# Kernel tuning notes

Hardware: AMD Instinct MI355X
Metric: run time of the kernel (lower is better)

Reference implementation:

```python
import jax, jax.numpy as jnp
import numpy as np

B, M, K, F, H = 4096, 50000, 31, 256, 256
N = K + 1                      # nodes per graph: center + K neighbors
GAMMA = 1.0 / (2.0 * 1.0 ** 2) # rbf_kernel gamma with length_scale = 1.0


def setup_inputs() -> dict:
    key = jax.random.key(0)
    k = jax.random.split(key, 9)
    return {
        "spatial_features": jax.random.normal(k[0], (B, 2), jnp.float32),
        "features": jax.random.normal(k[1], (B, F), jnp.float32),
        "train_spatial": jax.random.normal(k[2], (M, 2), jnp.float32),
        "train_features": jax.random.normal(k[3], (M, F), jnp.float32),
        "train_y": jax.random.normal(k[4], (M, 1), jnp.float32),
        "W0": jax.random.normal(k[5], (F + 2, H), jnp.float32) * (1.0 / np.sqrt(F + 2)),
        "W1": jax.random.normal(k[6], (H, H), jnp.float32) * (1.0 / np.sqrt(H)),
        "W2": jax.random.normal(k[7], (H, H), jnp.float32) * (1.0 / np.sqrt(H)),
        "Wout": jax.random.normal(k[8], (H, 1), jnp.float32) * (1.0 / np.sqrt(H)),
    }


def reference(spatial_features, features, train_spatial, train_features, train_y,
              W0, W1, W2, Wout):
    # --- brute-force kNN over train spatial coords (sklearn kneighbors) ---
    d2 = (jnp.sum(spatial_features ** 2, -1, keepdims=True)
          - 2.0 * spatial_features @ train_spatial.T
          + jnp.sum(train_spatial ** 2, -1)[None, :])                 # [B, M]
    nb = jax.lax.top_k(jax.lax.stop_gradient(-d2), K)[1]              # [B, K] indices

    # --- form_input_graph: node features = [feat ++ y ++ indicator] ---
    feat = jnp.concatenate([features[:, None, :], train_features[nb]], axis=1)    # [B,N,F]
    y = jnp.concatenate([jnp.zeros((B, 1, 1), feat.dtype), train_y[nb]], axis=1)  # [B,N,1]
    ind = jnp.zeros((B, N, 1), feat.dtype).at[:, 0, 0].set(1.0)                   # [B,N,1]
    x = jnp.concatenate([feat, y, ind], axis=-1)                                  # [B,N,F+2]

    # --- dense RBF adjacency: complete graph, self-loops already on diagonal ---
    coords = jnp.concatenate([spatial_features[:, None, :], train_spatial[nb]], axis=1)  # [B,N,2]
    diff = coords[:, :, None, :] - coords[:, None, :, :]
    A = jnp.exp(-GAMMA * jnp.sum(diff * diff, -1))                    # [B,N,N]
    # GCN symmetric normalization D^-1/2 A D^-1/2 (deg > 0 since diag = 1)
    dinv = jax.lax.rsqrt(jnp.sum(A, -1))                              # [B,N]
    Ahat = A * dinv[:, :, None] * dinv[:, None, :]

    h = jax.nn.relu(jnp.einsum('bij,bjh->bih', Ahat, x @ W0))
    h = jax.nn.relu(jnp.einsum('bij,bjh->bih', Ahat, h @ W1))
    h = jax.nn.relu(jnp.einsum('bij,bjh->bih', Ahat, h @ W2))

    # center node -> linear head (bias=False), last_activation='none'
    return h[:, 0] @ Wout                                             # [B, 1]
```

## Files before the change

kernel.cpp:

```cpp
#include <hip/hip_runtime.h>

typedef _Float16 half8 __attribute__((ext_vector_type(8)));
typedef float f32x16 __attribute__((ext_vector_type(16)));

#define M_TRAIN 50000
#define NQ 4096
#define KNN 31

#define LO_SCALE 1024.0f
#define LO_INV   9.765625e-4f

__global__ void prep_weights_k(const float* __restrict__ W0,
                               const float* __restrict__ W1,
                               const float* __restrict__ W2,
                               _Float16* __restrict__ W0hi, _Float16* __restrict__ W0lo,
                               _Float16* __restrict__ W1hi, _Float16* __restrict__ W1lo,
                               _Float16* __restrict__ W2hi, _Float16* __restrict__ W2lo) {
    int t = blockIdx.x * 256 + threadIdx.x;
    const int n0 = 17 * 8 * 64, n1 = 16 * 8 * 64, n2 = 16 * 8 * 64;
    if (t >= n0 + n1 + n2) return;
    const float* src; _Float16 *dhi, *dlo; int idx, Kin;
    if (t < n0)           { src = W0; dhi = W0hi; dlo = W0lo; idx = t;           Kin = 258; }
    else if (t < n0 + n1) { src = W1; dhi = W1hi; dlo = W1lo; idx = t - n0;      Kin = 256; }
    else                  { src = W2; dhi = W2hi; dlo = W2lo; idx = t - n0 - n1; Kin = 256; }
    int lane = idx & 63, nt = (idx >> 6) & 7, ks = idx >> 9;
    int col = nt * 32 + (lane & 31);
    int k0  = ks * 16 + (lane >> 5) * 8;
    _Float16 vhi[8], vlo[8];
#pragma unroll
    for (int j = 0; j < 8; j++) {
        int k = k0 + j;
        float w = (k < Kin) ? src[k * 256 + col] : 0.f;
        _Float16 hi = (_Float16)w;
        vhi[j] = hi;
        vlo[j] = (_Float16)((w - (float)hi) * LO_SCALE);
    }
    *reinterpret_cast<uint4*>(dhi + (size_t)idx * 8) = *reinterpret_cast<const uint4*>(vhi);
    *reinterpret_cast<uint4*>(dlo + (size_t)idx * 8) = *reinterpret_cast<const uint4*>(vlo);
}

#define QPB2 4
#define TILE2 2048
#define CAP2 128

__global__ __launch_bounds__(256) void knn_k(const float* __restrict__ qs,
                                             const float* __restrict__ ts,
                                             int* __restrict__ nb) {
    __shared__ __align__(16) float tile[TILE2 * 2];
    __shared__ float  mrg[QPB2][128];
    __shared__ int    ci[QPB2][CAP2];
    __shared__ double chd[QPB2][CAP2];
    __shared__ int    cnt[QPB2];

    const int t = threadIdx.x;
    const int w = t >> 6, lane = t & 63;
    const int q = blockIdx.x * QPB2 + w;

    if (lane == 0) cnt[w] = 0;
    const float qx = qs[q * 2 + 0], qy = qs[q * 2 + 1];

    float v0 = 3.4e38f, v1 = 3.4e38f;
    for (int base = 0; base < M_TRAIN; base += TILE2) {
        const int n = min(TILE2, M_TRAIN - base);
        __syncthreads();
        for (int i = t; i < n / 2; i += 256)
            reinterpret_cast<float4*>(tile)[i] =
                reinterpret_cast<const float4*>(ts + (size_t)base * 2)[i];
        __syncthreads();
#pragma unroll 4
        for (int p = lane; p < n; p += 64) {
            float dx = qx - tile[2 * p], dy = qy - tile[2 * p + 1];
            float d2 = dx * dx + dy * dy;
            if (d2 < v1) { if (d2 < v0) { v1 = v0; v0 = d2; } else v1 = d2; }
        }
    }
    __syncthreads();
    mrg[w][2 * lane]     = v0;
    mrg[w][2 * lane + 1] = v1;
    __syncthreads();

    float xa = mrg[w][lane], xb = mrg[w][64 + lane];
    int lea = 0, leb = 0;
    for (int i = 0; i < 128; i++) {
        float v = mrg[w][i];
        lea += (v <= xa) ? 1 : 0;
        leb += (v <= xb) ? 1 : 0;
    }
    float tc = 3.4e38f;
    if (lea >= 31) tc = xa;
    if (leb >= 31 && xb < tc) tc = xb;
#pragma unroll
    for (int off = 32; off; off >>= 1)
        tc = fminf(tc, __shfl_xor(tc, off));
    const float thr = tc * 1.00001f + 1e-7f;

    for (int base = 0; base < M_TRAIN; base += TILE2) {
        const int n = min(TILE2, M_TRAIN - base);
        __syncthreads();
        for (int i = t; i < n / 2; i += 256)
            reinterpret_cast<float4*>(tile)[i] =
                reinterpret_cast<const float4*>(ts + (size_t)base * 2)[i];
        __syncthreads();
#pragma unroll 4
        for (int p = lane; p < n; p += 64) {
            float dx = qx - tile[2 * p], dy = qy - tile[2 * p + 1];
            float d2 = dx * dx + dy * dy;
            if (d2 < thr) {
                int pos = atomicAdd(&cnt[w], 1);
                if (pos < CAP2) ci[w][pos] = base + p;
            }
        }
    }
    __syncthreads();

    const int C = min(cnt[w], CAP2);
    for (int c = lane; c < C; c += 64) {
        int idx = ci[w][c];
        double dx = (double)qx - (double)ts[idx * 2];
        double dy = (double)qy - (double)ts[idx * 2 + 1];
        chd[w][c] = dx * dx + dy * dy;
    }
    __syncthreads();
    for (int c = lane; c < C; c += 64) {
        double key = chd[w][c];
        int   idx = ci[w][c];
        int rank = 0;
        for (int o = 0; o < C; o++) {
            double ok = chd[w][o];
            int    oi = ci[w][o];
            rank += ((ok < key) || (ok == key && oi < idx)) ? 1 : 0;
        }
        if (rank < KNN) nb[q * KNN + rank] = idx;
    }
}

#define PX 276
#define PT 36

__device__ inline half8 ld_h8(const _Float16* p) {
    union { half8 h; uint2 u[2]; } r;
    r.u[0] = *reinterpret_cast<const uint2*>(p);
    r.u[1] = *reinterpret_cast<const uint2*>(p + 4);
    return r.h;
}
__device__ inline half8 ld_h8_g(const _Float16* p) {
    union { half8 h; uint4 u; } r;
    r.u = *reinterpret_cast<const uint4*>(p);
    return r.h;
}
__device__ inline f32x16 zero16() {
    f32x16 z;
#pragma unroll
    for (int i = 0; i < 16; i++) z[i] = 0.f;
    return z;
}
__device__ inline unsigned packh(_Float16 a, _Float16 b) {
    union { _Float16 f[2]; unsigned u; } p;
    p.f[0] = a; p.f[1] = b;
    return p.u;
}
__device__ inline half8 frag_x(const unsigned* w, int ks2, int h) {
    unsigned w0 = w[4 * ks2 + 0], w1 = w[4 * ks2 + 1];
    unsigned w2 = w[4 * ks2 + 2], w3 = w[4 * ks2 + 3];
    unsigned sA = h ? w0 : w2, sB = h ? w1 : w3;
    unsigned rA = __shfl_xor(sA, 32);
    unsigned rB = __shfl_xor(sB, 32);
    unsigned kA = h ? w2 : w0, kB = h ? w3 : w1;
    union { half8 h8; unsigned u[4]; } f;
    f.u[0] = h ? rA : kA;
    f.u[1] = h ? rB : kB;
    f.u[2] = h ? kA : rA;
    f.u[3] = h ? kB : rB;
    return f.h8;
}
#define MFMA(a, b, c) __builtin_amdgcn_mfma_f32_32x32x16_f16((a), (b), (c), 0, 0, 0)

__global__ __launch_bounds__(256, 4) void gcn_k(
    const float* __restrict__ qs, const float* __restrict__ qf,
    const float* __restrict__ ts, const float* __restrict__ tf,
    const float* __restrict__ ty, const float* __restrict__ Wout,
    const int* __restrict__ nb,
    const _Float16* __restrict__ W0hi, const _Float16* __restrict__ W0lo,
    const _Float16* __restrict__ W1hi, const _Float16* __restrict__ W1lo,
    const _Float16* __restrict__ W2hi, const _Float16* __restrict__ W2lo,
    float* __restrict__ out) {
    __shared__ __align__(16) _Float16 Xhi[32 * PX];
    __shared__ __align__(16) _Float16 Xlo[32 * PX];
    __shared__ _Float16 Ahhi[32 * PT];
    __shared__ _Float16 Ahlo[32 * PT];
    __shared__ float coords[64];
    __shared__ float dinv[32];
    __shared__ float yvs[32];
    __shared__ int   idxs[32];

    const int t = threadIdx.x;
    const int w = t >> 6, lane = t & 63;
    const int h = lane >> 5, ln = lane & 31;
    const int q0 = blockIdx.x;

    if (t < 32) {
        int idx = (t == 0) ? -1 : nb[q0 * KNN + (t - 1)];
        idxs[t] = idx;
        const float* c = (t == 0) ? (qs + (size_t)q0 * 2) : (ts + (size_t)idx * 2);
        coords[t * 2 + 0] = c[0];
        coords[t * 2 + 1] = c[1];
        yvs[t] = (t == 0) ? 0.f : ty[idx];
    }
    __syncthreads();

    {
        const float* src0 = (w == 0) ? (qf + (size_t)q0 * 256)
                                     : (tf + (size_t)idxs[w] * 256);
        float4 pv = reinterpret_cast<const float4*>(src0)[lane];
        for (int r = w; r < 32; r += 4) {
            float4 cv = pv;
            int rn = r + 4;
            if (rn < 32)
                pv = reinterpret_cast<const float4*>(tf + (size_t)idxs[rn] * 256)[lane];
            float a4[4] = {cv.x, cv.y, cv.z, cv.w};
            _Float16 hi4[4], lo4[4];
#pragma unroll
            for (int j = 0; j < 4; j++) {
                _Float16 hi = (_Float16)a4[j];
                hi4[j] = hi;
                lo4[j] = (_Float16)((a4[j] - (float)hi) * LO_SCALE);
            }
            *reinterpret_cast<uint2*>(&Xhi[r * PX + 4 * lane]) = *reinterpret_cast<uint2*>(hi4);
            *reinterpret_cast<uint2*>(&Xlo[r * PX + 4 * lane]) = *reinterpret_cast<uint2*>(lo4);
            if (lane == 0) {
                float yv = yvs[r];
                _Float16 thi[16], tlo[16];
#pragma unroll
                for (int j = 0; j < 16; j++) { thi[j] = (_Float16)0.f; tlo[j] = (_Float16)0.f; }
                _Float16 yh = (_Float16)yv;
                thi[0] = yh;
                tlo[0] = (_Float16)((yv - (float)yh) * LO_SCALE);
                thi[1] = (r == 0) ? (_Float16)1.f : (_Float16)0.f;
#pragma unroll
                for (int c = 0; c < 4; c++) {
                    *reinterpret_cast<uint2*>(&Xhi[r * PX + 256 + 4 * c]) = reinterpret_cast<uint2*>(thi)[c];
                    *reinterpret_cast<uint2*>(&Xlo[r * PX + 256 + 4 * c]) = reinterpret_cast<uint2*>(tlo)[c];
                }
            }
        }
    }

    if (t < 64) {
        int i = t >> 1, jh = t & 1;
        float xi = coords[i * 2], yi = coords[i * 2 + 1];
        float part = 0.f;
#pragma unroll
        for (int jj = 0; jj < 16; jj++) {
            int j = jh * 16 + jj;
            float dx = xi - coords[j * 2], dy = yi - coords[j * 2 + 1];
            part += __expf(-0.5f * (dx * dx + dy * dy));
        }
        float asum = part + __shfl_xor(part, 1);
        if (jh == 0) dinv[i] = 1.0f / sqrtf(asum);
    }
    __syncthreads();
    if (t < 64) {
        int i = t >> 1, jh = t & 1;
        float xi = coords[i * 2], yi = coords[i * 2 + 1];
        float di = dinv[i];
        _Float16 ahi[16], alo[16];
#pragma unroll
        for (int jj = 0; jj < 16; jj++) {
            int j = jh * 16 + jj;
            float dx = xi - coords[j * 2], dy = yi - coords[j * 2 + 1];
            float a = __expf(-0.5f * (dx * dx + dy * dy)) * di * dinv[j];
            _Float16 hi = (_Float16)a;
            ahi[jj] = hi;
            alo[jj] = (_Float16)((a - (float)hi) * LO_SCALE);
        }
        _Float16* dh = &Ahhi[i * PT + jh * 16];
        _Float16* dl = &Ahlo[i * PT + jh * 16];
#pragma unroll
        for (int c = 0; c < 4; c++) {
            reinterpret_cast<uint2*>(dh)[c] = reinterpret_cast<uint2*>(ahi)[c];
            reinterpret_cast<uint2*>(dl)[c] = reinterpret_cast<uint2*>(alo)[c];
        }
    }
    __syncthreads();

    const _Float16* Whis[3] = {W0hi, W1hi, W2hi};
    const _Float16* Wlos[3] = {W0lo, W1lo, W2lo};
    for (int layer = 0; layer < 3; layer++) {
        const _Float16* Whi = Whis[layer];
        const _Float16* Wlo = Wlos[layer];
        const int KS = (layer == 0) ? 17 : 16;

        f32x16 acc0 = zero16(), acc1 = zero16();
        f32x16 cor0 = zero16(), cor1 = zero16();
        size_t bo = ((size_t)(2 * w) * 64 + lane) * 8;
        half8 cAhi = ld_h8(&Xhi[ln * PX + 8 * h]);
        half8 cAlo = ld_h8(&Xlo[ln * PX + 8 * h]);
        half8 cBh0 = ld_h8_g(Whi + bo);
        half8 cBh1 = ld_h8_g(Whi + bo + 512);
        half8 cBl0 = ld_h8_g(Wlo + bo);
        half8 cBl1 = ld_h8_g(Wlo + bo + 512);
#pragma unroll 4
        for (int ks = 0; ks < KS; ks++) {
            half8 nAhi, nAlo, nBh0, nBh1, nBl0, nBl1;
            const bool more = (ks + 1 < KS);
            if (more) {
                size_t nbo = bo + 4096;
                nAhi = ld_h8(&Xhi[ln * PX + (ks + 1) * 16 + 8 * h]);
                nAlo = ld_h8(&Xlo[ln * PX + (ks + 1) * 16 + 8 * h]);
                nBh0 = ld_h8_g(Whi + nbo);
                nBh1 = ld_h8_g(Whi + nbo + 512);
                nBl0 = ld_h8_g(Wlo + nbo);
                nBl1 = ld_h8_g(Wlo + nbo + 512);
            }
            acc0 = MFMA(cAhi, cBh0, acc0);
            cor0 = MFMA(cAlo, cBh0, cor0);
            cor0 = MFMA(cAhi, cBl0, cor0);
            acc1 = MFMA(cAhi, cBh1, acc1);
            cor1 = MFMA(cAlo, cBh1, cor1);
            cor1 = MFMA(cAhi, cBl1, cor1);
            if (more) {
                cAhi = nAhi; cAlo = nAlo;
                cBh0 = nBh0; cBh1 = nBh1; cBl0 = nBl0; cBl1 = nBl1;
                bo += 4096;
            }
        }
        __syncthreads();

        unsigned whi0[8], wlo0[8], whi1[8], wlo1[8];
#pragma unroll
        for (int g = 0; g < 8; g++) {
            _Float16 ah[2], al[2], bh[2], bl[2];
#pragma unroll
            for (int e = 0; e < 2; e++) {
                int r = 2 * g + e;
                float x0 = acc0[r] + cor0[r] * LO_INV;
                _Float16 h0 = (_Float16)x0;
                ah[e] = h0; al[e] = (_Float16)((x0 - (float)h0) * LO_SCALE);
                float x1 = acc1[r] + cor1[r] * LO_INV;
                _Float16 h1 = (_Float16)x1;
                bh[e] = h1; bl[e] = (_Float16)((x1 - (float)h1) * LO_SCALE);
            }
            whi0[g] = packh(ah[0], ah[1]); wlo0[g] = packh(al[0], al[1]);
            whi1[g] = packh(bh[0], bh[1]); wlo1[g] = packh(bl[0], bl[1]);
        }

        f32x16 p0 = zero16(), p1 = zero16();
        f32x16 pc0 = zero16(), pc1 = zero16();
#pragma unroll
        for (int ks2 = 0; ks2 < 2; ks2++) {
            half8 bAhi = ld_h8(&Ahhi[ln * PT + ks2 * 16 + 8 * h]);
            half8 bAlo = ld_h8(&Ahlo[ln * PT + ks2 * 16 + 8 * h]);
            half8 t0hi = frag_x(whi0, ks2, h);
            half8 t0lo = frag_x(wlo0, ks2, h);
            half8 t1hi = frag_x(whi1, ks2, h);
            half8 t1lo = frag_x(wlo1, ks2, h);
            p0  = MFMA(t0hi, bAhi, p0);
            pc0 = MFMA(t0lo, bAhi, pc0);
            pc0 = MFMA(t0hi, bAlo, pc0);
            p1  = MFMA(t1hi, bAhi, p1);
            pc1 = MFMA(t1lo, bAhi, pc1);
            pc1 = MFMA(t1hi, bAlo, pc1);
        }

#pragma unroll
        for (int a = 0; a < 2; a++) {
            const f32x16& A = a ? p1 : p0;
            const f32x16& C = a ? pc1 : pc0;
#pragma unroll
            for (int c = 0; c < 4; c++) {
                _Float16 vh[4], vl[4];
#pragma unroll
                for (int m = 0; m < 4; m++) {
                    float x = A[4 * c + m] + C[4 * c + m] * LO_INV;
                    x = x > 0.f ? x : 0.f;
                    _Float16 hi = (_Float16)x;
                    vh[m] = hi;
                    vl[m] = (_Float16)((x - (float)hi) * LO_SCALE);
                }
                int feat = 64 * w + 32 * a + 8 * c + 4 * h;
                *reinterpret_cast<uint2*>(&Xhi[ln * PX + feat]) = *reinterpret_cast<uint2*>(vh);
                *reinterpret_cast<uint2*>(&Xlo[ln * PX + feat]) = *reinterpret_cast<uint2*>(vl);
            }
        }
        __syncthreads();
    }

    if (w == 0) {
        float4 wv = reinterpret_cast<const float4*>(Wout)[lane];
        union { uint2 u; _Float16 f[4]; } hh, hl;
        hh.u = *reinterpret_cast<const uint2*>(&Xhi[4 * lane]);
        hl.u = *reinterpret_cast<const uint2*>(&Xlo[4 * lane]);
        float s = ((float)hh.f[0] + (float)hl.f[0] * LO_INV) * wv.x
                + ((float)hh.f[1] + (float)hl.f[1] * LO_INV) * wv.y
                + ((float)hh.f[2] + (float)hl.f[2] * LO_INV) * wv.z
                + ((float)hh.f[3] + (float)hl.f[3] * LO_INV) * wv.w;
#pragma unroll
        for (int off = 32; off; off >>= 1) s += __shfl_xor(s, off);
        if (lane == 0) out[q0] = s;
    }
}

extern "C" void kernel_launch(void* const* d_in, const int* in_sizes, int n_in,
                              void* d_out, int out_size, void* d_ws, size_t ws_size,
                              hipStream_t stream) {
    const float* qs   = (const float*)d_in[0];
    const float* qf   = (const float*)d_in[1];
    const float* ts   = (const float*)d_in[2];
    const float* tf   = (const float*)d_in[3];
    const float* ty   = (const float*)d_in[4];
    const float* W0   = (const float*)d_in[5];
    const float* W1   = (const float*)d_in[6];
    const float* W2   = (const float*)d_in[7];
    const float* Wout = (const float*)d_in[8];
    float* out = (float*)d_out;

    char* ws = (char*)d_ws;
    int*      nb   = (int*)ws;
    _Float16* W0hi = (_Float16*)(ws + 524288);
    _Float16* W0lo = (_Float16*)(ws + 663552);
    _Float16* W1hi = (_Float16*)(ws + 802816);
    _Float16* W1lo = (_Float16*)(ws + 933888);
    _Float16* W2hi = (_Float16*)(ws + 1064960);
    _Float16* W2lo = (_Float16*)(ws + 1196032);

    hipLaunchKernelGGL(prep_weights_k, dim3(98), dim3(256), 0, stream,
                       W0, W1, W2, W0hi, W0lo, W1hi, W1lo, W2hi, W2lo);
    hipLaunchKernelGGL(knn_k, dim3(NQ / QPB2), dim3(256), 0, stream, qs, ts, nb);
    hipLaunchKernelGGL(gcn_k, dim3(NQ), dim3(256), 0, stream,
                       qs, qf, ts, tf, ty, Wout, nb,
                       W0hi, W0lo, W1hi, W1lo, W2hi, W2lo, out);
}
```

Before: 351.2 us.

## Use branchless kNN top-2, packed fp16 conversions, and simpler MFMA k-loop

In the kNN scan, each point is now read as a float2 and the running top-2 is kept with min/max instead of nested branches. Fp16 hi/lo splitting in the GCN kernel now uses the packed round-toward-zero convert intrinsic and fma for recombining the correction term. The manual software prefetch in the MFMA k-loop is removed in favour of direct loads with unroll 2, leaving scheduling to the compiler. The round-toward-zero convert changes rounding of the hi part, but the lo term should still absorb the residual; dropping the explicit prefetch may expose global load latency.

```diff
diff --git a/kernel.cpp b/kernel.cpp
--- a/kernel.cpp
+++ b/kernel.cpp
@@ -1,6 +1,7 @@
 #include <hip/hip_runtime.h>
 
 typedef _Float16 half8 __attribute__((ext_vector_type(8)));
+typedef __fp16  fp16x2 __attribute__((ext_vector_type(2)));
 typedef float f32x16 __attribute__((ext_vector_type(16)));
 
 #define M_TRAIN 50000
@@ -58,6 +59,7 @@
 
     if (lane == 0) cnt[w] = 0;
     const float qx = qs[q * 2 + 0], qy = qs[q * 2 + 1];
+    const float2* tilev = reinterpret_cast<const float2*>(tile);
 
     float v0 = 3.4e38f, v1 = 3.4e38f;
     for (int base = 0; base < M_TRAIN; base += TILE2) {
@@ -69,9 +71,11 @@
         __syncthreads();
 #pragma unroll 4
         for (int p = lane; p < n; p += 64) {
-            float dx = qx - tile[2 * p], dy = qy - tile[2 * p + 1];
-            float d2 = dx * dx + dy * dy;
-            if (d2 < v1) { if (d2 < v0) { v1 = v0; v0 = d2; } else v1 = d2; }
+            float2 pt = tilev[p];
+            float dx = qx - pt.x, dy = qy - pt.y;
+            float d2 = fmaf(dx, dx, dy * dy);
+            v1 = fminf(v1, fmaxf(v0, d2));
+            v0 = fminf(v0, d2);
         }
     }
     __syncthreads();
@@ -103,8 +107,9 @@
         __syncthreads();
 #pragma unroll 4
         for (int p = lane; p < n; p += 64) {
-            float dx = qx - tile[2 * p], dy = qy - tile[2 * p + 1];
-            float d2 = dx * dx + dy * dy;
+            float2 pt = tilev[p];
+            float dx = qx - pt.x, dy = qy - pt.y;
+            float d2 = fmaf(dx, dx, dy * dy);
             if (d2 < thr) {
                 int pos = atomicAdd(&cnt[w], 1);
                 if (pos < CAP2) ci[w][pos] = base + p;
@@ -154,10 +159,16 @@
     for (int i = 0; i < 16; i++) z[i] = 0.f;
     return z;
 }
-__device__ inline unsigned packh(_Float16 a, _Float16 b) {
-    union { _Float16 f[2]; unsigned u; } p;
-    p.f[0] = a; p.f[1] = b;
-    return p.u;
+__device__ inline unsigned pk_u(float a, float b) {
+    union { fp16x2 v; unsigned u; } c;
+    c.v = __builtin_amdgcn_cvt_pkrtz(a, b);
+    return c.u;
+}
+__device__ inline float f16lo(unsigned u) {
+    union { unsigned u; fp16x2 v; } c; c.u = u; return (float)c.v[0];
+}
+__device__ inline float f16hi(unsigned u) {
+    union { unsigned u; fp16x2 v; } c; c.u = u; return (float)c.v[1];
 }
 __device__ inline half8 frag_x(const unsigned* w, int ks2, int h) {
     unsigned w0 = w[4 * ks2 + 0], w1 = w[4 * ks2 + 1];
@@ -218,15 +229,16 @@
             if (rn < 32)
                 pv = reinterpret_cast<const float4*>(tf + (size_t)idxs[rn] * 256)[lane];
             float a4[4] = {cv.x, cv.y, cv.z, cv.w};
-            _Float16 hi4[4], lo4[4];
-#pragma unroll
-            for (int j = 0; j < 4; j++) {
-                _Float16 hi = (_Float16)a4[j];
-                hi4[j] = hi;
-                lo4[j] = (_Float16)((a4[j] - (float)hi) * LO_SCALE);
+            unsigned hw[2], lw[2];
+#pragma unroll
+            for (int j = 0; j < 2; j++) {
+                float x0 = a4[2 * j], x1 = a4[2 * j + 1];
+                hw[j] = pk_u(x0, x1);
+                lw[j] = pk_u((x0 - f16lo(hw[j])) * LO_SCALE,
+                             (x1 - f16hi(hw[j])) * LO_SCALE);
             }
-            *reinterpret_cast<uint2*>(&Xhi[r * PX + 4 * lane]) = *reinterpret_cast<uint2*>(hi4);
-            *reinterpret_cast<uint2*>(&Xlo[r * PX + 4 * lane]) = *reinterpret_cast<uint2*>(lo4);
+            *reinterpret_cast<uint2*>(&Xhi[r * PX + 4 * lane]) = *reinterpret_cast<uint2*>(hw);
+            *reinterpret_cast<uint2*>(&Xlo[r * PX + 4 * lane]) = *reinterpret_cast<uint2*>(lw);
             if (lane == 0) {
                 float yv = yvs[r];
                 _Float16 thi[16], tlo[16];
@@ -292,56 +304,40 @@
 
         f32x16 acc0 = zero16(), acc1 = zero16();
         f32x16 cor0 = zero16(), cor1 = zero16();
-        size_t bo = ((size_t)(2 * w) * 64 + lane) * 8;
-        half8 cAhi = ld_h8(&Xhi[ln * PX + 8 * h]);
-        half8 cAlo = ld_h8(&Xlo[ln * PX + 8 * h]);
-        half8 cBh0 = ld_h8_g(Whi + bo);
-        half8 cBh1 = ld_h8_g(Whi + bo + 512);
-        half8 cBl0 = ld_h8_g(Wlo + bo);
-        half8 cBl1 = ld_h8_g(Wlo + bo + 512);
-#pragma unroll 4
+        const int boBase = (2 * w * 64 + lane) * 8;
+        const _Float16* Xa = &Xhi[ln * PX + 8 * h];
+        const _Float16* Xb = &Xlo[ln * PX + 8 * h];
+#pragma unroll 2
         for (int ks = 0; ks < KS; ks++) {
-            half8 nAhi, nAlo, nBh0, nBh1, nBl0, nBl1;
-            const bool more = (ks + 1 < KS);
-            if (more) {
-                size_t nbo = bo + 4096;
-                nAhi = ld_h8(&Xhi[ln * PX + (ks + 1) * 16 + 8 * h]);
-                nAlo = ld_h8(&Xlo[ln * PX + (ks + 1) * 16 + 8 * h]);
-                nBh0 = ld_h8_g(Whi + nbo);
-                nBh1 = ld_h8_g(Whi + nbo + 512);
-                nBl0 = ld_h8_g(Wlo + nbo);
-                nBl1 = ld_h8_g(Wlo + nbo + 512);
-            }
-            acc0 = MFMA(cAhi, cBh0, acc0);
-            cor0 = MFMA(cAlo, cBh0, cor0);
-            cor0 = MFMA(cAhi, cBl0, cor0);
-            acc1 = MFMA(cAhi, cBh1, acc1);
-            cor1 = MFMA(cAlo, cBh1, cor1);
-            cor1 = MFMA(cAhi, cBl1, cor1);
-            if (more) {
-                cAhi = nAhi; cAlo = nAlo;
-                cBh0 = nBh0; cBh1 = nBh1; cBl0 = nBl0; cBl1 = nBl1;
-                bo += 4096;
-            }
+            half8 Ahi_ = ld_h8(Xa + ks * 16);
+            half8 Alo_ = ld_h8(Xb + ks * 16);
+            int bo = boBase + ks * 4096;
+            half8 Bh0 = ld_h8_g(Whi + bo);
+            half8 Bh1 = ld_h8_g(Whi + bo + 512);
+            half8 Bl0 = ld_h8_g(Wlo + bo);
+            half8 Bl1 = ld_h8_g(Wlo + bo + 512);
+            acc0 = MFMA(Ahi_, Bh0, acc0);
+            cor0 = MFMA(Alo_, Bh0, cor0);
+            cor0 = MFMA(Ahi_, Bl0, cor0);
+            acc1 = MFMA(Ahi_, Bh1, acc1);
+            cor1 = MFMA(Alo_, Bh1, cor1);
+            cor1 = MFMA(Ahi_, Bl1, cor1);
         }
         __syncthreads();
 
         unsigned whi0[8], wlo0[8], whi1[8], wlo1[8];
 #pragma unroll
         for (int g = 0; g < 8; g++) {
-            _Float16 ah[2], al[2], bh[2], bl[2];
-#pragma unroll
-            for (int e = 0; e < 2; e++) {
-                int r = 2 * g + e;
-                float x0 = acc0[r] + cor0[r] * LO_INV;
-                _Float16 h0 = (_Float16)x0;
-                ah[e] = h0; al[e] = (_Float16)((x0 - (float)h0) * LO_SCALE);
-                float x1 = acc1[r] + cor1[r] * LO_INV;
-                _Float16 h1 = (_Float16)x1;
-                bh[e] = h1; bl[e] = (_Float16)((x1 - (float)h1) * LO_SCALE);
-            }
-            whi0[g] = packh(ah[0], ah[1]); wlo0[g] = packh(al[0], al[1]);
-            whi1[g] = packh(bh[0], bh[1]); wlo1[g] = packh(bl[0], bl[1]);
+            float x0 = fmaf(cor0[2 * g],     LO_INV, acc0[2 * g]);
+            float x1 = fmaf(cor0[2 * g + 1], LO_INV, acc0[2 * g + 1]);
+            unsigned hw = pk_u(x0, x1);
+            whi0[g] = hw;
+            wlo0[g] = pk_u((x0 - f16lo(hw)) * LO_SCALE, (x1 - f16hi(hw)) * LO_SCALE);
+            float y0 = fmaf(cor1[2 * g],     LO_INV, acc1[2 * g]);
+            float y1 = fmaf(cor1[2 * g + 1], LO_INV, acc1[2 * g + 1]);
+            unsigned hv = pk_u(y0, y1);
+            whi1[g] = hv;
+            wlo1[g] = pk_u((y0 - f16lo(hv)) * LO_SCALE, (y1 - f16hi(hv)) * LO_SCALE);
         }
 
         f32x16 p0 = zero16(), p1 = zero16();
@@ -368,18 +364,20 @@
             const f32x16& C = a ? pc1 : pc0;
 #pragma unroll
             for (int c = 0; c < 4; c++) {
-                _Float16 vh[4], vl[4];
-#pragma unroll
-                for (int m = 0; m < 4; m++) {
-                    float x = A[4 * c + m] + C[4 * c + m] * LO_INV;
-                    x = x > 0.f ? x : 0.f;
-                    _Float16 hi = (_Float16)x;
-                    vh[m] = hi;
-                    vl[m] = (_Float16)((x - (float)hi) * LO_SCALE);
-                }
+                float x0 = fmaf(C[4 * c + 0], LO_INV, A[4 * c + 0]);
+                float x1 = fmaf(C[4 * c + 1], LO_INV, A[4 * c + 1]);
+                float x2 = fmaf(C[4 * c + 2], LO_INV, A[4 * c + 2]);
+                float x3 = fmaf(C[4 * c + 3], LO_INV, A[4 * c + 3]);
+                x0 = fmaxf(x0, 0.f); x1 = fmaxf(x1, 0.f);
+                x2 = fmaxf(x2, 0.f); x3 = fmaxf(x3, 0.f);
+                unsigned hw[2], lw[2];
+                hw[0] = pk_u(x0, x1);
+                hw[1] = pk_u(x2, x3);
+                lw[0] = pk_u((x0 - f16lo(hw[0])) * LO_SCALE, (x1 - f16hi(hw[0])) * LO_SCALE);
+                lw[1] = pk_u((x2 - f16lo(hw[1])) * LO_SCALE, (x3 - f16hi(hw[1])) * LO_SCALE);
                 int feat = 64 * w + 32 * a + 8 * c + 4 * h;
-                *reinterpret_cast<uint2*>(&Xhi[ln * PX + feat]) = *reinterpret_cast<uint2*>(vh);
-                *reinterpret_cast<uint2*>(&Xlo[ln * PX + feat]) = *reinterpret_cast<uint2*>(vl);
+                *reinterpret_cast<uint2*>(&Xhi[ln * PX + feat]) = *reinterpret_cast<uint2*>(hw);
+                *reinterpret_cast<uint2*>(&Xlo[ln * PX + feat]) = *reinterpret_cast<uint2*>(lw);
             }
         }
         __syncthreads();
```

Result: faster. 327.9 us (-6.6%).
